# Kernel optimization log

Measured on AMD Instinct MI355X. Metric: run time of the kernel, lower is better.

Reference implementation:

```python
import jax, jax.numpy as jnp
import numpy as np

N_PER_GRAPH = 1024
BATCH = 32
N = N_PER_GRAPH * BATCH  # 32768 total nodes
E = 262144               # edges per edge set (before self loops)
EMB = 128
D = 128
NEG_SLOPE = 0.2


def setup_inputs() -> dict:
    key = jax.random.key(0)
    ks = jax.random.split(key, 20)
    def lin(k, i, o):
        return (jax.random.normal(k, (i, o), jnp.float32) / np.float32(np.sqrt(i)))
    inp = {}
    inp["x"] = jax.random.normal(ks[0], (N, EMB), jnp.float32)
    inp["edge_index_n"] = jax.random.randint(ks[1], (2, E), 0, N, jnp.int32)
    inp["edge_index_r0"] = jax.random.randint(ks[2], (2, E), 0, N, jnp.int32)
    inp["edge_index_r1"] = jax.random.randint(ks[3], (2, E), 0, N, jnp.int32)
    # gat_0: Linear(EMB->D) + attn Linear(2D->D)
    inp["W0_lin"] = lin(ks[4], EMB, D); inp["b0_lin"] = jnp.zeros((D,), jnp.float32)
    inp["W0_att"] = lin(ks[5], 2 * D, D); inp["b0_att"] = jnp.zeros((D,), jnp.float32)
    # gat_1 (shared, used twice)
    inp["W1_lin"] = lin(ks[6], D, D); inp["b1_lin"] = jnp.zeros((D,), jnp.float32)
    inp["W1_att"] = lin(ks[7], 2 * D, D); inp["b1_att"] = jnp.zeros((D,), jnp.float32)
    # gat_2 (shared, used twice)
    inp["W2_lin"] = lin(ks[8], D, D); inp["b2_lin"] = jnp.zeros((D,), jnp.float32)
    inp["W2_att"] = lin(ks[9], 2 * D, D); inp["b2_att"] = jnp.zeros((D,), jnp.float32)
    # lin_prob: Linear(D->1)
    inp["Wp"] = lin(ks[10], D, 1); inp["bp"] = jnp.zeros((1,), jnp.float32)
    # Attention: W1, W2 (D->D, no bias), vt (D->1, no bias)
    inp["Wa1"] = lin(ks[11], D, D)
    inp["Wa2"] = lin(ks[12], D, D)
    inp["vt"] = lin(ks[13], D, 1)
    return inp


def _gat(x, edge_index, Wl, bl, Wa, ba):
    """One GATConv: add self loops, lin, edge gather, attn MLP, segment softmax, scatter-add."""
    n = x.shape[0]
    loop = jnp.arange(n, dtype=edge_index.dtype)
    src = jnp.concatenate([edge_index[0], loop])  # x_j index
    dst = jnp.concatenate([edge_index[1], loop])  # x_i / aggregation index
    h = x @ Wl + bl                               # [N, D]
    hi = h[dst]                                   # [E+N, D]
    hj = h[src]                                   # [E+N, D]
    a = jnp.concatenate([hi, hj], axis=-1) @ Wa + ba  # [E+N, D]
    a = jax.nn.leaky_relu(a, NEG_SLOPE)
    # segment softmax over destination neighborhoods (vector-valued, per channel)
    m = jax.lax.stop_gradient(jax.ops.segment_max(a, dst, num_segments=n))
    ex = jnp.exp(a - m[dst])
    s = jax.ops.segment_sum(ex, dst, num_segments=n)
    alpha = ex / (s[dst] + 1e-16)
    return jax.ops.segment_sum(hj * alpha, dst, num_segments=n)


def reference(x, edge_index_n, edge_index_r0, edge_index_r1,
              W0_lin, b0_lin, W0_att, b0_att,
              W1_lin, b1_lin, W1_att, b1_att,
              W2_lin, b2_lin, W2_att, b2_att,
              Wp, bp, Wa1, Wa2, vt):
    g0 = _gat(x,  edge_index_n,  W0_lin, b0_lin, W0_att, b0_att)
    g1 = _gat(g0, edge_index_r1, W1_lin, b1_lin, W1_att, b1_att)
    g2 = _gat(g1, edge_index_r0, W2_lin, b2_lin, W2_att, b2_att)
    g3 = _gat(g2, edge_index_r1, W1_lin, b1_lin, W1_att, b1_att)
    g4 = _gat(g3, edge_index_r0, W2_lin, b2_lin, W2_att, b2_att)
    X = g4.reshape(BATCH, N_PER_GRAPH, D)
    h = X.mean(axis=1)                                       # [B, D]
    logits1 = (X @ Wp + bp).reshape(BATCH, N_PER_GRAPH)      # [B, n]
    prob1 = jax.nn.softmax(logits1[:, 1:], axis=-1)          # [B, n-1]
    k1, k2 = jax.random.split(jax.random.key(42))
    index1 = 1 + jax.random.categorical(k1, logits1[:, 1:], axis=-1)  # [B]
    b_ar = jnp.arange(BATCH)
    sampled = X[b_ar, index1][:, None, :]                    # [B, 1, D]
    u = (jnp.tanh(sampled @ Wa1 + X @ Wa2) @ vt)[..., 0]      # [B, n]
    u = u.at[b_ar, index1].set(-jnp.inf)
    prob2 = jax.nn.softmax(u[:, 1:], axis=-1)                # [B, n-1]
    index2 = 1 + jax.random.categorical(k2, u[:, 1:], axis=-1)
    probs = prob1[b_ar, index1 - 1] + prob2[b_ar, index2 - 1]
    log_probs = jnp.log(probs)
    return (h, index1, index2, log_probs)
```

## Files before the change

kernel.cpp:

```cpp
#include <hip/hip_runtime.h>
#include <stdint.h>
#include <math.h>

#define NN 32768
#define EE 262144
#define DD 128
#define NPG 1024
#define NB 32
#define NEG_SLOPE 0.2f
#define USE_PARTITIONABLE 1

__host__ __device__ inline void tf2x32(uint32_t k0, uint32_t k1, uint32_t c0, uint32_t c1,
                                       uint32_t* o0, uint32_t* o1) {
  uint32_t ks2 = k0 ^ k1 ^ 0x1BD11BDAu;
  uint32_t x0 = c0 + k0;
  uint32_t x1 = c1 + k1;
#define TFR(r) { x0 += x1; x1 = (x1 << (r)) | (x1 >> (32 - (r))); x1 ^= x0; }
  TFR(13) TFR(15) TFR(26) TFR(6)
  x0 += k1; x1 += ks2 + 1u;
  TFR(17) TFR(29) TFR(16) TFR(24)
  x0 += ks2; x1 += k0 + 2u;
  TFR(13) TFR(15) TFR(26) TFR(6)
  x0 += k0; x1 += k1 + 3u;
  TFR(17) TFR(29) TFR(16) TFR(24)
  x0 += k1; x1 += ks2 + 4u;
  TFR(13) TFR(15) TFR(26) TFR(6)
  x0 += ks2; x1 += k0 + 5u;
#undef TFR
  *o0 = x0; *o1 = x1;
}

__device__ inline float gumbel_from_bits(uint32_t bits) {
  float fl = __uint_as_float((bits >> 9) | 0x3f800000u) - 1.0f;
  const float tiny = 1.17549435e-38f;
  float u = fmaxf(tiny, fl + tiny);
  return -logf(-logf(u));
}

__device__ inline float gumbel_at(uint32_t ka, uint32_t kb, uint32_t f) {
#if USE_PARTITIONABLE
  uint32_t o0, o1;
  tf2x32(ka, kb, 0u, f, &o0, &o1);
  return gumbel_from_bits(o0 ^ o1);
#else
  const uint32_t HALF = 16368u;
  uint32_t o0, o1;
  if (f < HALF) { tf2x32(ka, kb, f, f + HALF, &o0, &o1); return gumbel_from_bits(o0); }
  else          { tf2x32(ka, kb, f - HALF, f, &o0, &o1); return gumbel_from_bits(o1); }
#endif
}

__global__ __launch_bounds__(256) void hist3_kernel(const int* __restrict__ e0,
                                                    const int* __restrict__ e1,
                                                    const int* __restrict__ e2,
                                                    int* __restrict__ counts3) {
  int s = blockIdx.x >> 10;
  int i = (blockIdx.x & 1023) * 256 + threadIdx.x;
  const int* d = (s == 0) ? e0 : (s == 1) ? e1 : e2;
  atomicAdd(&counts3[s * NN + d[i + EE]], 1);
}

__global__ __launch_bounds__(1024) void scan3_kernel(const int* __restrict__ counts3,
                                                     int* __restrict__ rowptrAll,
                                                     int* __restrict__ cursorAll) {
  __shared__ int part[1024];
  int s = blockIdx.x;
  const int* counts = counts3 + s * NN;
  int* rowptr = rowptrAll + s * (NN + 1);
  int* cursor = cursorAll + s * NN;
  int t = threadIdx.x;
  int base = t * 32;
  int local[32];
  {
    const int4* c4 = (const int4*)(counts + base);
    int sum = 0;
#pragma unroll
    for (int v = 0; v < 8; v++) {
      int4 cc = c4[v];
      local[v * 4 + 0] = sum; sum += cc.x;
      local[v * 4 + 1] = sum; sum += cc.y;
      local[v * 4 + 2] = sum; sum += cc.z;
      local[v * 4 + 3] = sum; sum += cc.w;
    }
    part[t] = sum;
  }
  __syncthreads();
  int own = part[t];
  for (int off = 1; off < 1024; off <<= 1) {
    int v = (t >= off) ? part[t - off] : 0;
    __syncthreads();
    part[t] += v;
    __syncthreads();
  }
  int excl = part[t] - own;
  {
    int4* rp4 = (int4*)(rowptr + base);
    int4* cu4 = (int4*)(cursor + base);
#pragma unroll
    for (int v = 0; v < 8; v++) {
      int4 w;
      w.x = excl + local[v * 4 + 0];
      w.y = excl + local[v * 4 + 1];
      w.z = excl + local[v * 4 + 2];
      w.w = excl + local[v * 4 + 3];
      rp4[v] = w;
      cu4[v] = w;
    }
  }
  if (t == 1023) rowptr[NN] = part[1023];
}

__global__ __launch_bounds__(256) void scatter3_kernel(const int* __restrict__ e0,
                                                       const int* __restrict__ e1,
                                                       const int* __restrict__ e2,
                                                       int* __restrict__ cursorAll,
                                                       int* __restrict__ colAll) {
  int s = blockIdx.x >> 10;
  int i = (blockIdx.x & 1023) * 256 + threadIdx.x;
  const int* e = (s == 0) ? e0 : (s == 1) ? e1 : e2;
  int src = e[i], dst = e[i + EE];
  int p = atomicAdd(&cursorAll[s * NN + dst], 1);
  colAll[(size_t)s * EE + p] = src;
}

#define FMA4(ac, s, v) { ac.x += (s) * (v).x; ac.y += (s) * (v).y; \
                         ac.z += (s) * (v).z; ac.w += (s) * (v).w; }

__global__ __launch_bounds__(256) void gemm8_kernel(const float* __restrict__ in,
                                                    const float* __restrict__ W,
                                                    const float* __restrict__ bias,
                                                    float* __restrict__ out) {
  __shared__ __align__(16) float at[2][16 * 132];
  __shared__ __align__(16) float ws[2][16 * 128];
  int t = threadIdx.x;
  size_t row0 = (size_t)blockIdx.x * 128;
  int tr = t >> 4, tcg = t & 15;
  int r0 = tr * 8;
  float4 acc0[8], acc1[8];
#pragma unroll
  for (int i = 0; i < 8; i++) {
    acc0[i] = make_float4(0.f, 0.f, 0.f, 0.f);
    acc1[i] = make_float4(0.f, 0.f, 0.f, 0.f);
  }
  int srow = t >> 2;
  int sc4 = (t & 3) * 4;
  int kkA = t >> 5;
  int jgA = (t & 31) * 4;

  float4 a0, a1, w0, w1;
  auto load_chunk = [&](int k0) {
    a0 = *(const float4*)&in[(row0 + srow) * DD + k0 + sc4];
    a1 = *(const float4*)&in[(row0 + srow + 64) * DD + k0 + sc4];
    w0 = *(const float4*)&W[(size_t)(k0 + kkA) * DD + jgA];
    w1 = *(const float4*)&W[(size_t)(k0 + kkA + 8) * DD + jgA];
  };
  auto write_chunk = [&](int b) {
    float* A = at[b];
    A[(sc4 + 0) * 132 + srow] = a0.x;
    A[(sc4 + 1) * 132 + srow] = a0.y;
    A[(sc4 + 2) * 132 + srow] = a0.z;
    A[(sc4 + 3) * 132 + srow] = a0.w;
    A[(sc4 + 0) * 132 + srow + 64] = a1.x;
    A[(sc4 + 1) * 132 + srow + 64] = a1.y;
    A[(sc4 + 2) * 132 + srow + 64] = a1.z;
    A[(sc4 + 3) * 132 + srow + 64] = a1.w;
    float* Wd = ws[b];
    *(float4*)&Wd[kkA * 128 + jgA] = w0;
    *(float4*)&Wd[(kkA + 8) * 128 + jgA] = w1;
  };

  load_chunk(0);
  write_chunk(0);
  __syncthreads();
  for (int kc = 0; kc < 8; ++kc) {
    int cur = kc & 1;
    if (kc < 7) load_chunk((kc + 1) * 16);
    const float* A = at[cur];
    const float* Wd = ws[cur];
#pragma unroll
    for (int kk = 0; kk < 16; ++kk) {
      float4 av0 = *(const float4*)&A[kk * 132 + r0];
      float4 av1 = *(const float4*)&A[kk * 132 + r0 + 4];
      float4 wv0 = *(const float4*)&Wd[kk * 128 + 4 * tcg];
      float4 wv1 = *(const float4*)&Wd[kk * 128 + 4 * tcg + 64];
      FMA4(acc0[0], av0.x, wv0); FMA4(acc1[0], av0.x, wv1);
      FMA4(acc0[1], av0.y, wv0); FMA4(acc1[1], av0.y, wv1);
      FMA4(acc0[2], av0.z, wv0); FMA4(acc1[2], av0.z, wv1);
      FMA4(acc0[3], av0.w, wv0); FMA4(acc1[3], av0.w, wv1);
      FMA4(acc0[4], av1.x, wv0); FMA4(acc1[4], av1.x, wv1);
      FMA4(acc0[5], av1.y, wv0); FMA4(acc1[5], av1.y, wv1);
      FMA4(acc0[6], av1.z, wv0); FMA4(acc1[6], av1.z, wv1);
      FMA4(acc0[7], av1.w, wv0); FMA4(acc1[7], av1.w, wv1);
    }
    if (kc < 7) {
      write_chunk(cur ^ 1);
    }
    __syncthreads();
  }
  float4 b0 = make_float4(0.f, 0.f, 0.f, 0.f), b1 = b0;
  if (bias) {
    b0 = *(const float4*)&bias[4 * tcg];
    b1 = *(const float4*)&bias[4 * tcg + 64];
  }
#pragma unroll
  for (int i = 0; i < 8; i++) {
    float4 o0 = acc0[i], o1 = acc1[i];
    o0.x += b0.x; o0.y += b0.y; o0.z += b0.z; o0.w += b0.w;
    o1.x += b1.x; o1.y += b1.y; o1.z += b1.z; o1.w += b1.w;
    *(float4*)&out[(row0 + r0 + i) * DD + 4 * tcg] = o0;
    *(float4*)&out[(row0 + r0 + i) * DD + 4 * tcg + 64] = o1;
  }
}

__device__ inline float lk1(float v) { return v > 0.f ? v : NEG_SLOPE * v; }

__global__ __launch_bounds__(256, 4) void gat_edge_kernel(const float* __restrict__ P,
                                                          const float* __restrict__ Q,
                                                          const float* __restrict__ H,
                                                          const int* __restrict__ rowptr,
                                                          const int* __restrict__ col,
                                                          float* __restrict__ out) {
  int wv = threadIdx.x >> 6;
  int lane = threadIdx.x & 63;
  int dst = (blockIdx.x << 2) + wv;
  int rs = __builtin_amdgcn_readfirstlane(rowptr[dst]);
  int re = __builtin_amdgcn_readfirstlane(rowptr[dst + 1]);
  int deg = re - rs;
  int total = deg + 1;
  float2 pd = ((const float2*)(P + (size_t)dst * DD))[lane];

  float mx = -INFINITY, my = -INFINITY;
  float sx = 0.f, sy = 0.f;
  float cx = 0.f, cy = 0.f;

  for (int base = 0; base < total; base += 64) {
    int cnt = min(64, total - base);
    int e = base + lane;
    int myidx = (e < deg) ? col[rs + e] : dst;
    int i = 0;
    for (; i + 4 <= cnt; i += 4) {
      int iu = __builtin_amdgcn_readfirstlane(i);
      int n0 = __builtin_amdgcn_readlane(myidx, iu);
      int n1 = __builtin_amdgcn_readlane(myidx, iu + 1);
      int n2 = __builtin_amdgcn_readlane(myidx, iu + 2);
      int n3 = __builtin_amdgcn_readlane(myidx, iu + 3);
      float2 q0 = ((const float2*)(Q + (size_t)n0 * DD))[lane];
      float2 q1 = ((const float2*)(Q + (size_t)n1 * DD))[lane];
      float2 q2 = ((const float2*)(Q + (size_t)n2 * DD))[lane];
      float2 q3 = ((const float2*)(Q + (size_t)n3 * DD))[lane];
      float2 h0 = ((const float2*)(H + (size_t)n0 * DD))[lane];
      float2 h1 = ((const float2*)(H + (size_t)n1 * DD))[lane];
      float2 h2 = ((const float2*)(H + (size_t)n2 * DD))[lane];
      float2 h3 = ((const float2*)(H + (size_t)n3 * DD))[lane];
      float a0x = lk1(pd.x + q0.x), a0y = lk1(pd.y + q0.y);
      float a1x = lk1(pd.x + q1.x), a1y = lk1(pd.y + q1.y);
      float a2x = lk1(pd.x + q2.x), a2y = lk1(pd.y + q2.y);
      float a3x = lk1(pd.x + q3.x), a3y = lk1(pd.y + q3.y);
      float nmx = fmaxf(fmaxf(mx, fmaxf(a0x, a1x)), fmaxf(a2x, a3x));
      float nmy = fmaxf(fmaxf(my, fmaxf(a0y, a1y)), fmaxf(a2y, a3y));
      float scx = expf(mx - nmx), scy = expf(my - nmy);
      float e0x = expf(a0x - nmx), e1x = expf(a1x - nmx);
      float e2x = expf(a2x - nmx), e3x = expf(a3x - nmx);
      float e0y = expf(a0y - nmy), e1y = expf(a1y - nmy);
      float e2y = expf(a2y - nmy), e3y = expf(a3y - nmy);
      sx = sx * scx + ((e0x + e1x) + (e2x + e3x));
      sy = sy * scy + ((e0y + e1y) + (e2y + e3y));
      cx = cx * scx + ((e0x * h0.x + e1x * h1.x) + (e2x * h2.x + e3x * h3.x));
      cy = cy * scy + ((e0y * h0.y + e1y * h1.y) + (e2y * h2.y + e3y * h3.y));
      mx = nmx; my = nmy;
    }
    for (; i < cnt; i++) {
      int iu = __builtin_amdgcn_readfirstlane(i);
      int n0 = __builtin_amdgcn_readlane(myidx, iu);
      float2 q0 = ((const float2*)(Q + (size_t)n0 * DD))[lane];
      float2 h0 = ((const float2*)(H + (size_t)n0 * DD))[lane];
      float a0x = lk1(pd.x + q0.x), a0y = lk1(pd.y + q0.y);
      float nmx = fmaxf(mx, a0x), nmy = fmaxf(my, a0y);
      float scx = expf(mx - nmx), scy = expf(my - nmy);
      float e0x = expf(a0x - nmx), e0y = expf(a0y - nmy);
      sx = sx * scx + e0x;
      sy = sy * scy + e0y;
      cx = cx * scx + e0x * h0.x;
      cy = cy * scy + e0y * h0.y;
      mx = nmx; my = nmy;
    }
  }
  float2 o = make_float2(cx / (sx + 1e-16f), cy / (sy + 1e-16f));
  ((float2*)(out + (size_t)dst * DD))[lane] = o;
}

__global__ __launch_bounds__(256) void logits_kernel(const float* __restrict__ X,
                                                     const float* __restrict__ Wp,
                                                     const float* __restrict__ bp,
                                                     float* __restrict__ logits) {
  int w = threadIdx.x >> 6, lane = threadIdx.x & 63;
  int n = blockIdx.x * 4 + w;
  const float* xr = X + (size_t)n * DD;
  float p = xr[lane] * Wp[lane] + xr[lane + 64] * Wp[lane + 64];
  for (int off = 32; off > 0; off >>= 1) p += __shfl_down(p, off);
  if (lane == 0) logits[n] = p + bp[0];
}

__global__ __launch_bounds__(1024) void hmean_kernel(const float* __restrict__ X,
                                                     float* __restrict__ out) {
  int b = blockIdx.x;
  int t = threadIdx.x;
  int c = t & 127, part = t >> 7;
  float acc = 0.f;
  for (int i = part; i < NPG; i += 8)
    acc += X[((size_t)b * NPG + i) * DD + c];
  __shared__ float red[1024];
  red[t] = acc; __syncthreads();
  if (part == 0) {
    float s = 0.f;
#pragma unroll
    for (int p = 0; p < 8; p++) s += red[p * 128 + c];
    out[b * DD + c] = s * (1.0f / (float)NPG);
  }
}

__global__ __launch_bounds__(256) void sample1_kernel(const float* __restrict__ logits,
                                                      uint32_t ka, uint32_t kb,
                                                      int* __restrict__ idx1_ws,
                                                      float* __restrict__ p1_ws,
                                                      float* __restrict__ out) {
  int b = blockIdx.x, t = threadIdx.x;
  __shared__ float sV[256]; __shared__ int sJ[256]; __shared__ float sM[256];
  float bestV = -INFINITY; int bestJ = 1 << 30; float maxL = -INFINITY;
  for (int j = 1 + t; j < NPG; j += 256) {
    float l = logits[(size_t)b * NPG + j];
    maxL = fmaxf(maxL, l);
    float v = l + gumbel_at(ka, kb, (uint32_t)(b * 1023 + j - 1));
    if (v > bestV) { bestV = v; bestJ = j; }
  }
  sV[t] = bestV; sJ[t] = bestJ; sM[t] = maxL; __syncthreads();
  for (int off = 128; off > 0; off >>= 1) {
    if (t < off) {
      if (sV[t + off] > sV[t] || (sV[t + off] == sV[t] && sJ[t + off] < sJ[t])) {
        sV[t] = sV[t + off]; sJ[t] = sJ[t + off];
      }
      sM[t] = fmaxf(sM[t], sM[t + off]);
    }
    __syncthreads();
  }
  float M = sM[0]; int idx = sJ[0];
  __syncthreads();
  float ps = 0.f;
  for (int j = 1 + t; j < NPG; j += 256)
    ps += expf(logits[(size_t)b * NPG + j] - M);
  sV[t] = ps; __syncthreads();
  for (int off = 128; off > 0; off >>= 1) {
    if (t < off) sV[t] += sV[t + off];
    __syncthreads();
  }
  if (t == 0) {
    float S = sV[0];
    float p1 = expf(logits[(size_t)b * NPG + idx] - M) / S;
    idx1_ws[b] = idx;
    p1_ws[b] = p1;
    out[NB * DD + b] = (float)idx;
  }
}

__global__ __launch_bounds__(128) void zk_kernel(const float* __restrict__ X,
                                                 const float* __restrict__ Wa1,
                                                 const int* __restrict__ idx1,
                                                 float* __restrict__ Z) {
  int b = blockIdx.x, c = threadIdx.x;
  __shared__ float xs[128];
  int node = b * NPG + idx1[b];
  xs[c] = X[(size_t)node * DD + c];
  __syncthreads();
  float acc = 0.f;
#pragma unroll 8
  for (int k = 0; k < 128; k++) acc += xs[k] * Wa1[k * 128 + c];
  Z[b * DD + c] = acc;
}

__global__ __launch_bounds__(256) void u_kernel(const float* __restrict__ Y,
                                                const float* __restrict__ Z,
                                                const float* __restrict__ vt,
                                                const int* __restrict__ idx1,
                                                float* __restrict__ u) {
  int w = threadIdx.x >> 6, lane = threadIdx.x & 63;
  int n = blockIdx.x * 4 + w;
  int b = n >> 10;
  float t0 = tanhf(Z[b * DD + lane] + Y[(size_t)n * DD + lane]) * vt[lane];
  float t1 = tanhf(Z[b * DD + lane + 64] + Y[(size_t)n * DD + lane + 64]) * vt[lane + 64];
  float p = t0 + t1;
  for (int off = 32; off > 0; off >>= 1) p += __shfl_down(p, off);
  if (lane == 0) u[n] = ((n & (NPG - 1)) == idx1[b]) ? -INFINITY : p;
}

__global__ __launch_bounds__(256) void sample2_kernel(const float* __restrict__ u,
                                                      uint32_t ka, uint32_t kb,
                                                      const float* __restrict__ p1_ws,
                                                      float* __restrict__ out) {
  int b = blockIdx.x, t = threadIdx.x;
  __shared__ float sV[256]; __shared__ int sJ[256]; __shared__ float sM[256];
  float bestV = -INFINITY; int bestJ = 1 << 30; float maxL = -INFINITY;
  for (int j = 1 + t; j < NPG; j += 256) {
    float l = u[(size_t)b * NPG + j];
    maxL = fmaxf(maxL, l);
    float v = l + gumbel_at(ka, kb, (uint32_t)(b * 1023 + j - 1));
    if (v > bestV) { bestV = v; bestJ = j; }
  }
  sV[t] = bestV; sJ[t] = bestJ; sM[t] = maxL; __syncthreads();
  for (int off = 128; off > 0; off >>= 1) {
    if (t < off) {
      if (sV[t + off] > sV[t] || (sV[t + off] == sV[t] && sJ[t + off] < sJ[t])) {
        sV[t] = sV[t + off]; sJ[t] = sJ[t + off];
      }
      sM[t] = fmaxf(sM[t], sM[t + off]);
    }
    __syncthreads();
  }
  float M = sM[0]; int idx = sJ[0];
  __syncthreads();
  float ps = 0.f;
  for (int j = 1 + t; j < NPG; j += 256) {
    float l = u[(size_t)b * NPG + j];
    ps += expf(l - M);
  }
  sV[t] = ps; __syncthreads();
  for (int off = 128; off > 0; off >>= 1) {
    if (t < off) sV[t] += sV[t + off];
    __syncthreads();
  }
  if (t == 0) {
    float S = sV[0];
    float p2 = expf(u[(size_t)b * NPG + idx] - M) / S;
    out[NB * DD + NB + b] = (float)idx;
    out[NB * DD + 2 * NB + b] = logf(p1_ws[b] + p2);
  }
}

extern "C" void kernel_launch(void* const* d_in, const int* in_sizes, int n_in,
                              void* d_out, int out_size, void* d_ws, size_t ws_size,
                              hipStream_t stream) {
  const float* x  = (const float*)d_in[0];
  const int* eN   = (const int*)d_in[1];
  const int* eR0  = (const int*)d_in[2];
  const int* eR1  = (const int*)d_in[3];
  const float* W0l = (const float*)d_in[4];  const float* b0l = (const float*)d_in[5];
  const float* W0a = (const float*)d_in[6];  const float* b0a = (const float*)d_in[7];
  const float* W1l = (const float*)d_in[8];  const float* b1l = (const float*)d_in[9];
  const float* W1a = (const float*)d_in[10]; const float* b1a = (const float*)d_in[11];
  const float* W2l = (const float*)d_in[12]; const float* b2l = (const float*)d_in[13];
  const float* W2a = (const float*)d_in[14]; const float* b2a = (const float*)d_in[15];
  const float* Wp  = (const float*)d_in[16]; const float* bp  = (const float*)d_in[17];
  const float* Wa1 = (const float*)d_in[18]; const float* Wa2 = (const float*)d_in[19];
  const float* vt  = (const float*)d_in[20];
  float* out = (float*)d_out;

  char* wsb = (char*)d_ws;
  size_t off = 0;
  auto take = [&](size_t bytes) -> char* {
    char* p = wsb + off;
    off += (bytes + 255) & ~(size_t)255;
    return p;
  };
  int* rowptrAll = (int*)take((size_t)3 * (NN + 1) * sizeof(int));
  int* counts3   = (int*)take((size_t)3 * NN * sizeof(int));
  int* cursorAll = (int*)take((size_t)3 * NN * sizeof(int));
  int* colAll    = (int*)take((size_t)3 * EE * sizeof(int));
  float* bufA    = (float*)take((size_t)NN * DD * 4);
  float* bufB    = (float*)take((size_t)NN * DD * 4);
  float* hb      = (float*)take((size_t)NN * DD * 4);
  float* Pb      = (float*)take((size_t)NN * DD * 4);
  float* Qb      = (float*)take((size_t)NN * DD * 4);
  float* logits  = (float*)take((size_t)NN * 4);
  float* ub      = (float*)take((size_t)NN * 4);
  float* Zb      = (float*)take((size_t)NB * DD * 4);
  int* idx1b     = (int*)take(NB * 4);
  float* p1b     = (float*)take(NB * 4);

  uint32_t k1a, k1b, k2a, k2b;
#if USE_PARTITIONABLE
  {
    uint32_t o0, o1;
    tf2x32(0u, 42u, 0u, 0u, &o0, &o1); k1a = o0; k1b = o1;
    tf2x32(0u, 42u, 0u, 1u, &o0, &o1); k2a = o0; k2b = o1;
  }
#else
  {
    uint32_t a0, b0, a1, b1;
    tf2x32(0u, 42u, 0u, 2u, &a0, &b0);
    tf2x32(0u, 42u, 1u, 3u, &a1, &b1);
    k1a = a0; k1b = a1; k2a = b0; k2b = b1;
  }
#endif

  hipMemsetAsync(counts3, 0, (size_t)3 * NN * sizeof(int), stream);
  hist3_kernel<<<3 * 1024, 256, 0, stream>>>(eN, eR0, eR1, counts3);
  scan3_kernel<<<3, 1024, 0, stream>>>(counts3, rowptrAll, cursorAll);
  scatter3_kernel<<<3 * 1024, 256, 0, stream>>>(eN, eR0, eR1, cursorAll, colAll);

  struct Layer { const float* in; float* o; const float *Wl, *bl, *Wa, *ba; int set; };
  Layer Ls[5] = {
      {x,    bufA, W0l, b0l, W0a, b0a, 0},
      {bufA, bufB, W1l, b1l, W1a, b1a, 2},
      {bufB, bufA, W2l, b2l, W2a, b2a, 1},
      {bufA, bufB, W1l, b1l, W1a, b1a, 2},
      {bufB, bufA, W2l, b2l, W2a, b2a, 1},
  };
  for (int L = 0; L < 5; L++) {
    gemm8_kernel<<<NN / 128, 256, 0, stream>>>(Ls[L].in, Ls[L].Wl, Ls[L].bl, hb);
    gemm8_kernel<<<NN / 128, 256, 0, stream>>>(hb, Ls[L].Wa, Ls[L].ba, Pb);
    gemm8_kernel<<<NN / 128, 256, 0, stream>>>(hb, Ls[L].Wa + 128 * 128, nullptr, Qb);
    gat_edge_kernel<<<NN / 4, 256, 0, stream>>>(
        Pb, Qb, hb, rowptrAll + Ls[L].set * (NN + 1),
        colAll + (size_t)Ls[L].set * EE, Ls[L].o);
  }
  const float* X = bufA;

  gemm8_kernel<<<NN / 128, 256, 0, stream>>>(X, Wa2, nullptr, Pb);
  logits_kernel<<<NN / 4, 256, 0, stream>>>(X, Wp, bp, logits);
  hmean_kernel<<<NB, 1024, 0, stream>>>(X, out);
  sample1_kernel<<<NB, 256, 0, stream>>>(logits, k1a, k1b, idx1b, p1b, out);
  zk_kernel<<<NB, 128, 0, stream>>>(X, Wa1, idx1b, Zb);
  u_kernel<<<NN / 4, 256, 0, stream>>>(Pb, Zb, vt, idx1b, ub);
  sample2_kernel<<<NB, 256, 0, stream>>>(ub, k2a, k2b, p1b, out);
}
```

Baseline: 837.7 us.

## Precompose linear and attention weights into one fused 384-wide GEMM per layer

Folds Wl into the two halves of the attention weight matrix up front, so each layer computes h, P and Q from its input in a single GEMM against a 128x384 combined weight, with biases composed in a small bbig kernel. This replaces three dependent 128-wide GEMM launches per layer, removing the write and reread of h between them and two launches. In exchange each block holds 24 float4 accumulators, so register pressure rises and occupancy may fall, and the results round slightly differently because the weight product is reassociated.

After: 778.4 us. 1.08x faster.

```diff
diff --git a/kernel.cpp b/kernel.cpp
--- a/kernel.cpp
+++ b/kernel.cpp
@@ -125,6 +125,174 @@
 
 #define FMA4(ac, s, v) { ac.x += (s) * (v).x; ac.y += (s) * (v).y; \
                          ac.z += (s) * (v).z; ac.w += (s) * (v).w; }
+
+__global__ __launch_bounds__(256) void wbig_kernel(const float* __restrict__ W0l,
+                                                   const float* __restrict__ W0a,
+                                                   const float* __restrict__ W1l,
+                                                   const float* __restrict__ W1a,
+                                                   const float* __restrict__ W2l,
+                                                   const float* __restrict__ W2a,
+                                                   float* __restrict__ WbigAll) {
+  int s = blockIdx.x >> 4, rb = blockIdx.x & 15;
+  const float* Wl = (s == 0) ? W0l : (s == 1) ? W1l : W2l;
+  const float* Wa = (s == 0) ? W0a : (s == 1) ? W1a : W2a;
+  float* Wbig = WbigAll + (size_t)s * 128 * 384;
+  __shared__ float wl[8][128];
+  __shared__ float wa[16][256];
+  int t = threadIdx.x;
+  {
+    int r = t >> 5, c4 = (t & 31) * 4;
+    float4 v = *(const float4*)&Wl[(size_t)(rb * 8 + r) * 128 + c4];
+    *(float4*)&wl[r][c4] = v;
+    *(float4*)&Wbig[(size_t)(rb * 8 + r) * 384 + c4] = v;
+  }
+  __syncthreads();
+  int r = t >> 5, cg = t & 31;
+  float4 accT = make_float4(0.f, 0.f, 0.f, 0.f);
+  float4 accB = make_float4(0.f, 0.f, 0.f, 0.f);
+  for (int kc = 0; kc < 8; ++kc) {
+    int k0 = kc * 16;
+#pragma unroll
+    for (int i = 0; i < 4; ++i) {
+      int g = t + 256 * i;
+      int kk = g >> 6, c4g = g & 63;
+      const float* src = (c4g < 32)
+          ? &Wa[(size_t)(k0 + kk) * 128 + c4g * 4]
+          : &Wa[(size_t)(128 + k0 + kk) * 128 + (c4g - 32) * 4];
+      *(float4*)&wa[kk][c4g * 4] = *(const float4*)src;
+    }
+    __syncthreads();
+#pragma unroll
+    for (int kk = 0; kk < 16; ++kk) {
+      float a = wl[r][k0 + kk];
+      float4 wt = *(const float4*)&wa[kk][4 * cg];
+      float4 wb = *(const float4*)&wa[kk][128 + 4 * cg];
+      FMA4(accT, a, wt);
+      FMA4(accB, a, wb);
+    }
+    __syncthreads();
+  }
+  *(float4*)&Wbig[(size_t)(rb * 8 + r) * 384 + 128 + 4 * cg] = accT;
+  *(float4*)&Wbig[(size_t)(rb * 8 + r) * 384 + 256 + 4 * cg] = accB;
+}
+
+__global__ __launch_bounds__(128) void bbig_kernel(const float* __restrict__ b0l,
+                                                   const float* __restrict__ b0a,
+                                                   const float* __restrict__ W0a,
+                                                   const float* __restrict__ b1l,
+                                                   const float* __restrict__ b1a,
+                                                   const float* __restrict__ W1a,
+                                                   const float* __restrict__ b2l,
+                                                   const float* __restrict__ b2a,
+                                                   const float* __restrict__ W2a,
+                                                   float* __restrict__ bbigAll) {
+  int s = blockIdx.x, c = threadIdx.x;
+  const float* bl = (s == 0) ? b0l : (s == 1) ? b1l : b2l;
+  const float* ba = (s == 0) ? b0a : (s == 1) ? b1a : b2a;
+  const float* Wa = (s == 0) ? W0a : (s == 1) ? W1a : W2a;
+  __shared__ float blS[128];
+  blS[c] = bl[c];
+  __syncthreads();
+  float aT = 0.f, aB = 0.f;
+  for (int k = 0; k < 128; ++k) {
+    aT += blS[k] * Wa[(size_t)k * 128 + c];
+    aB += blS[k] * Wa[(size_t)(128 + k) * 128 + c];
+  }
+  float* bb = bbigAll + s * 384;
+  bb[c] = blS[c];
+  bb[128 + c] = aT + ba[c];
+  bb[256 + c] = aB;
+}
+
+__global__ __launch_bounds__(256) void fused384_kernel(const float* __restrict__ in,
+                                                       const float* __restrict__ Wbig,
+                                                       const float* __restrict__ bbig,
+                                                       float* __restrict__ h,
+                                                       float* __restrict__ P,
+                                                       float* __restrict__ Q) {
+  __shared__ __align__(16) float at[2][16 * 68];
+  __shared__ __align__(16) float wsb[2][16 * 384];
+  int t = threadIdx.x;
+  size_t row0 = (size_t)blockIdx.x * 64;
+  int rowg = t >> 5, cg = t & 31;
+  int r0 = rowg * 8;
+  float4 acc0[8], acc1[8], acc2[8];
+#pragma unroll
+  for (int i = 0; i < 8; i++) {
+    acc0[i] = make_float4(0.f, 0.f, 0.f, 0.f);
+    acc1[i] = make_float4(0.f, 0.f, 0.f, 0.f);
+    acc2[i] = make_float4(0.f, 0.f, 0.f, 0.f);
+  }
+  int srow = t >> 2, sc4 = (t & 3) * 4;
+  int wkk[6], wc4[6];
+#pragma unroll
+  for (int i = 0; i < 6; i++) {
+    int g = t + 256 * i;
+    wkk[i] = g / 96;
+    wc4[i] = (g % 96) * 4;
+  }
+  float4 aR;
+  float4 wR[6];
+  auto load_chunk = [&](int k0) {
+    aR = *(const float4*)&in[(row0 + srow) * DD + k0 + sc4];
+#pragma unroll
+    for (int i = 0; i < 6; i++)
+      wR[i] = *(const float4*)&Wbig[(size_t)(k0 + wkk[i]) * 384 + wc4[i]];
+  };
+  auto write_chunk = [&](int b) {
+    float* A = at[b];
+    A[(sc4 + 0) * 68 + srow] = aR.x;
+    A[(sc4 + 1) * 68 + srow] = aR.y;
+    A[(sc4 + 2) * 68 + srow] = aR.z;
+    A[(sc4 + 3) * 68 + srow] = aR.w;
+    float* Wd = wsb[b];
+#pragma unroll
+    for (int i = 0; i < 6; i++)
+      *(float4*)&Wd[wkk[i] * 384 + wc4[i]] = wR[i];
+  };
+
+  load_chunk(0);
+  write_chunk(0);
+  __syncthreads();
+  for (int kc = 0; kc < 8; ++kc) {
+    int cur = kc & 1;
+    if (kc < 7) load_chunk((kc + 1) * 16);
+    const float* A = at[cur];
+    const float* Wd = wsb[cur];
+#pragma unroll 4
+    for (int kk = 0; kk < 16; ++kk) {
+      float4 av0 = *(const float4*)&A[kk * 68 + r0];
+      float4 av1 = *(const float4*)&A[kk * 68 + r0 + 4];
+      float4 wv0 = *(const float4*)&Wd[kk * 384 + 4 * cg];
+      float4 wv1 = *(const float4*)&Wd[kk * 384 + 4 * cg + 128];
+      float4 wv2 = *(const float4*)&Wd[kk * 384 + 4 * cg + 256];
+      FMA4(acc0[0], av0.x, wv0); FMA4(acc1[0], av0.x, wv1); FMA4(acc2[0], av0.x, wv2);
+      FMA4(acc0[1], av0.y, wv0); FMA4(acc1[1], av0.y, wv1); FMA4(acc2[1], av0.y, wv2);
+      FMA4(acc0[2], av0.z, wv0); FMA4(acc1[2], av0.z, wv1); FMA4(acc2[2], av0.z, wv2);
+      FMA4(acc0[3], av0.w, wv0); FMA4(acc1[3], av0.w, wv1); FMA4(acc2[3], av0.w, wv2);
+      FMA4(acc0[4], av1.x, wv0); FMA4(acc1[4], av1.x, wv1); FMA4(acc2[4], av1.x, wv2);
+      FMA4(acc0[5], av1.y, wv0); FMA4(acc1[5], av1.y, wv1); FMA4(acc2[5], av1.y, wv2);
+      FMA4(acc0[6], av1.z, wv0); FMA4(acc1[6], av1.z, wv1); FMA4(acc2[6], av1.z, wv2);
+      FMA4(acc0[7], av1.w, wv0); FMA4(acc1[7], av1.w, wv1); FMA4(acc2[7], av1.w, wv2);
+    }
+    if (kc < 7) write_chunk(cur ^ 1);
+    __syncthreads();
+  }
+  float4 b0 = *(const float4*)&bbig[4 * cg];
+  float4 b1 = *(const float4*)&bbig[128 + 4 * cg];
+  float4 b2 = *(const float4*)&bbig[256 + 4 * cg];
+#pragma unroll
+  for (int i = 0; i < 8; i++) {
+    size_t orow = (row0 + r0 + i) * DD + 4 * cg;
+    float4 o0 = acc0[i], o1 = acc1[i], o2 = acc2[i];
+    o0.x += b0.x; o0.y += b0.y; o0.z += b0.z; o0.w += b0.w;
+    o1.x += b1.x; o1.y += b1.y; o1.z += b1.z; o1.w += b1.w;
+    o2.x += b2.x; o2.y += b2.y; o2.z += b2.z; o2.w += b2.w;
+    *(float4*)&h[orow] = o0;
+    *(float4*)&P[orow] = o1;
+    *(float4*)&Q[orow] = o2;
+  }
+}
 
 __global__ __launch_bounds__(256) void gemm8_kernel(const float* __restrict__ in,
                                                     const float* __restrict__ W,
@@ -192,9 +360,7 @@
       FMA4(acc0[6], av1.z, wv0); FMA4(acc1[6], av1.z, wv1);
       FMA4(acc0[7], av1.w, wv0); FMA4(acc1[7], av1.w, wv1);
     }
-    if (kc < 7) {
-      write_chunk(cur ^ 1);
-    }
+    if (kc < 7) write_chunk(cur ^ 1);
     __syncthreads();
   }
   float4 b0 = make_float4(0.f, 0.f, 0.f, 0.f), b1 = b0;
@@ -474,6 +640,8 @@
   float* Zb      = (float*)take((size_t)NB * DD * 4);
   int* idx1b     = (int*)take(NB * 4);
   float* p1b     = (float*)take(NB * 4);
+  float* WbigAll = (float*)take((size_t)3 * 128 * 384 * 4);
+  float* bbigAll = (float*)take((size_t)3 * 384 * 4);
 
   uint32_t k1a, k1b, k2a, k2b;
 #if USE_PARTITIONABLE
@@ -491,23 +659,25 @@
   }
 #endif
 
+  wbig_kernel<<<48, 256, 0, stream>>>(W0l, W0a, W1l, W1a, W2l, W2a, WbigAll);
+  bbig_kernel<<<3, 128, 0, stream>>>(b0l, b0a, W0a, b1l, b1a, W1a, b2l, b2a, W2a, bbigAll);
   hipMemsetAsync(counts3, 0, (size_t)3 * NN * sizeof(int), stream);
   hist3_kernel<<<3 * 1024, 256, 0, stream>>>(eN, eR0, eR1, counts3);
   scan3_kernel<<<3, 1024, 0, stream>>>(counts3, rowptrAll, cursorAll);
   scatter3_kernel<<<3 * 1024, 256, 0, stream>>>(eN, eR0, eR1, cursorAll, colAll);
 
-  struct Layer { const float* in; float* o; const float *Wl, *bl, *Wa, *ba; int set; };
+  struct Layer { const float* in; float* o; int type; int set; };
   Layer Ls[5] = {
-      {x,    bufA, W0l, b0l, W0a, b0a, 0},
-      {bufA, bufB, W1l, b1l, W1a, b1a, 2},
-      {bufB, bufA, W2l, b2l, W2a, b2a, 1},
-      {bufA, bufB, W1l, b1l, W1a, b1a, 2},
-      {bufB, bufA, W2l, b2l, W2a, b2a, 1},
+      {x,    bufA, 0, 0},
+      {bufA, bufB, 1, 2},
+      {bufB, bufA, 2, 1},
+      {bufA, bufB, 1, 2},
+      {bufB, bufA, 2, 1},
   };
   for (int L = 0; L < 5; L++) {
-    gemm8_kernel<<<NN / 128, 256, 0, stream>>>(Ls[L].in, Ls[L].Wl, Ls[L].bl, hb);
-    gemm8_kernel<<<NN / 128, 256, 0, stream>>>(hb, Ls[L].Wa, Ls[L].ba, Pb);
-    gemm8_kernel<<<NN / 128, 256, 0, stream>>>(hb, Ls[L].Wa + 128 * 128, nullptr, Qb);
+    fused384_kernel<<<NN / 64, 256, 0, stream>>>(
+        Ls[L].in, WbigAll + (size_t)Ls[L].type * 128 * 384,
+        bbigAll + (size_t)Ls[L].type * 384, hb, Pb, Qb);
     gat_edge_kernel<<<NN / 4, 256, 0, stream>>>(
         Pb, Qb, hb, rowptrAll + Ls[L].set * (NN + 1),
         colAll + (size_t)Ls[L].set * EE, Ls[L].o);
```
